# Performance work log

Hardware: AMD Instinct MI355X
Metric: run time of the kernel (lower is better)

The kernel has to match this reference:

```python
import jax, jax.numpy as jnp
import numpy as np


def setup_inputs() -> dict:
    key = jax.random.key(0)
    k1, k2 = jax.random.split(key)
    B, C, H, W = 4, 64, 256, 256
    x = jax.random.normal(k1, (B, C, H, W), dtype=jnp.float32)
    perspective = jax.random.uniform(k2, (B, 1, H, W), dtype=jnp.float32)
    alpha = jnp.ones((1,), dtype=jnp.float32) * 3.0   # sigma scale
    beta = jnp.ones((1,), dtype=jnp.float32)          # sigmoid slope
    gamma = jnp.zeros((1,), dtype=jnp.float32)        # sigmoid shift
    return {"x": x, "perspective": perspective, "alpha": alpha,
            "beta": beta, "gamma": gamma, "kernel_size": 7}


def reference(x, perspective, alpha, beta, gamma, kernel_size):
    K = int(kernel_size)
    pad = K // 2
    B, C, H, W = x.shape
    # AdaptiveSigmoid sigma map, clamped like the torch module
    sigma = jnp.maximum(alpha * jax.nn.sigmoid(beta * perspective + gamma), 1e-4)  # [B,1,H,W]
    inv2s2 = 1.0 / (2.0 * sigma * sigma)                                           # [B,1,H,W]
    # squared distance of each kernel tap from center (static)
    offs = np.arange(K) - pad
    d2 = (offs[:, None] ** 2 + offs[None, :] ** 2).reshape(-1).astype(np.float32)  # [K*K]
    # per-pixel, per-tap Gaussian weights, normalized over taps
    w = jnp.exp(-d2[:, None, None, None, None] * inv2s2[None])  # [K*K,B,1,H,W]
    w = w / jnp.sum(w, axis=0)
    xp = jnp.pad(x, ((0, 0), (0, 0), (pad, pad), (pad, pad)))
    out = jnp.zeros_like(x)
    k = 0
    for i in range(K):            # fixed small K*K loop (49 taps), jit-friendly
        for j in range(K):
            out = out + w[k] * xp[:, :, i:i + H, j:j + W]
            k += 1
    return out
```

## Files before the change

### kernel.cpp

```cpp
#include <hip/hip_runtime.h>

#define NB 4
#define NC 64
#define NH 256
#define NW 256
#define TH 32
#define SROWS (TH + 6)
#define LROW 256

__global__ __launch_bounds__(256)
void wprep(const float* __restrict__ persp,
           const float* __restrict__ alpha_p,
           const float* __restrict__ beta_p,
           const float* __restrict__ gamma_p,
           float* __restrict__ wg)
{
    const float alpha = alpha_p[0];
    const float beta  = beta_p[0];
    const float gamma = gamma_p[0];
    const int i = (blockIdx.x * 256 + threadIdx.x) * 4;
    const float4 p = *(const float4*)(persp + i);
    const float pa[4] = {p.x, p.y, p.z, p.w};
    float g[4];
    #pragma unroll
    for (int k = 0; k < 4; ++k) {
        const float z  = fmaf(beta, pa[k], gamma);
        const float sg = __builtin_amdgcn_rcpf(1.0f + __expf(-z));
        const float sigma = fmaxf(alpha * sg, 1e-4f);
        const float t  = 0.5f * __builtin_amdgcn_rcpf(sigma * sigma);
        g[k] = __expf(-t);
    }
    *(float4*)(wg + i) = make_float4(g[0], g[1], g[2], g[3]);
}

__device__ __forceinline__ float dpp_shr1(float v) {
    return __int_as_float(__builtin_amdgcn_update_dpp(
        0, __float_as_int(v), 0x138 , 0xf, 0xf, true));
}
__device__ __forceinline__ float dpp_shl1(float v) {
    return __int_as_float(__builtin_amdgcn_update_dpp(
        0, __float_as_int(v), 0x130 , 0xf, 0xf, true));
}

__global__ __launch_bounds__(256, 3)
void adaptive_gauss7(const float* __restrict__ x,
                     const float* __restrict__ wgp,
                     float* __restrict__ out)
{
    __shared__ float lds[SROWS * LROW];

    const int tid  = threadIdx.x;
    const int lane = tid & 63;
    const int wv   = tid >> 6;
    const int c    = blockIdx.x;
    const int h0   = blockIdx.y * TH;
    const int b    = blockIdx.z;
    const int colbase = lane * 4;
    const int rg      = h0 + wv * 8;

    const float* xc   = x   + (size_t)(b * NC + c) * NH * NW;
    float*       outp = out + (size_t)(b * NC + c) * NH * NW;
    const float* wrow = wgp + (size_t)b * NH * NW;

    float4 wsg[8];
    #pragma unroll
    for (int o = 0; o < 8; ++o)
        wsg[o] = *(const float4*)(wrow + (size_t)(rg + o) * NW + colbase);

    for (int r = wv; r < SROWS; r += 4) {
        const int gr = h0 - 3 + r;
        if ((unsigned)gr < NH) {
            __builtin_amdgcn_global_load_lds(
                (const __attribute__((address_space(1))) void*)(xc + (size_t)gr * NW + colbase),
                (__attribute__((address_space(3))) void*)&lds[r * LROW],
                16, 0, 0);
        } else {
            *(float4*)&lds[r * LROW + colbase] = make_float4(0.f, 0.f, 0.f, 0.f);
        }
    }
    __syncthreads();

    float win[7][4];
    #pragma unroll
    for (int r = 0; r < 7; ++r) {
        const float4 a = *(const float4*)&lds[(wv * 8 + r) * LROW + colbase];
        win[r][0] = a.x; win[r][1] = a.y; win[r][2] = a.z; win[r][3] = a.w;
    }

    #pragma unroll
    for (int o = 0; o < 8; ++o) {
        const float gk[4] = {wsg[o].x, wsg[o].y, wsg[o].z, wsg[o].w};
        float g[4], p4[4], p9[4], inv2[4];
        #pragma unroll
        for (int k = 0; k < 4; ++k) {
            g[k] = gk[k];
            const float g2 = g[k] * g[k];
            p4[k] = g2 * g2;
            p9[k] = p4[k] * p4[k] * g[k];
            const float S  = fmaf(2.0f, (g[k] + p4[k]) + p9[k], 1.0f);
            const float iv = __builtin_amdgcn_rcpf(S);
            inv2[k] = iv * iv;
        }

        float s0[4], s1[4], s2[4], s3[4];
        #pragma unroll
        for (int j = 0; j < 7; ++j) {
            const int s = (o + j) % 7;
            const float w[10] = {
                dpp_shr1(win[s][1]),
                dpp_shr1(win[s][2]),
                dpp_shr1(win[s][3]),
                win[s][0], win[s][1], win[s][2], win[s][3],
                dpp_shl1(win[s][0]),
                dpp_shl1(win[s][1]),
                dpp_shl1(win[s][2])
            };
            #pragma unroll
            for (int k = 0; k < 4; ++k) {
                const float rs = fmaf(p9[k], w[k]     + w[k + 6],
                                 fmaf(p4[k], w[k + 1] + w[k + 5],
                                 fmaf(g[k],  w[k + 2] + w[k + 4],
                                             w[k + 3])));
                if      (j == 0) s0[k] = rs;
                else if (j == 1) s1[k] = rs;
                else if (j == 2) s2[k] = rs;
                else if (j == 3) s3[k] = rs;
                else if (j == 4) s2[k] = s2[k] + rs;
                else if (j == 5) s1[k] = s1[k] + rs;
                else             s0[k] = s0[k] + rs;
            }
        }

        float res[4];
        #pragma unroll
        for (int k = 0; k < 4; ++k) {
            res[k] = fmaf(p9[k], s0[k],
                     fmaf(p4[k], s1[k],
                     fmaf(g[k],  s2[k], s3[k]))) * inv2[k];
        }
        *(float4*)(outp + (size_t)(rg + o) * NW + colbase) =
            make_float4(res[0], res[1], res[2], res[3]);

        if (o < 7) {
            const float4 a = *(const float4*)&lds[(wv * 8 + o + 7) * LROW + colbase];
            win[o % 7][0] = a.x; win[o % 7][1] = a.y;
            win[o % 7][2] = a.z; win[o % 7][3] = a.w;
        }
    }
}

extern "C" void kernel_launch(void* const* d_in, const int* in_sizes, int n_in,
                              void* d_out, int out_size, void* d_ws, size_t ws_size,
                              hipStream_t stream) {
    const float* x     = (const float*)d_in[0];
    const float* persp = (const float*)d_in[1];
    const float* alpha = (const float*)d_in[2];
    const float* beta  = (const float*)d_in[3];
    const float* gamma = (const float*)d_in[4];
    float* outp        = (float*)d_out;
    float* wg          = (float*)d_ws;

    wprep<<<dim3((NB * NH * NW) / 1024), dim3(256), 0, stream>>>(persp, alpha, beta, gamma, wg);
    adaptive_gauss7<<<dim3(NC, NH / TH, NB), dim3(256), 0, stream>>>(x, wg, outp);
}
```

Measured before the change: 136.1 us.

## Process several channels per block with double-buffered LDS staging

Each block now handles four channels instead of one. The next channel's tile is staged into a second LDS buffer with async global-to-LDS loads while the current channel is computed. The per-pixel Gaussian weights are loaded once and reused across those channels, which cuts redundant weight loads and per-block launch overhead. In exchange, LDS per block doubles, which limits blocks per CU, and the grid shrinks to a quarter as many blocks. The compiler may also insert conservative waits that serialize the prefetch.

```diff
diff --git a/kernel.cpp b/kernel.cpp
--- a/kernel.cpp
+++ b/kernel.cpp
@@ -4,6 +4,7 @@
 #define NC 64
 #define NH 256
 #define NW 256
+#define CPB 4
 #define TH 32
 #define SROWS (TH + 6)
 #define LROW 256
@@ -47,104 +48,118 @@
                      const float* __restrict__ wgp,
                      float* __restrict__ out)
 {
-    __shared__ float lds[SROWS * LROW];
+    __shared__ float lds[2][SROWS * LROW];
 
     const int tid  = threadIdx.x;
     const int lane = tid & 63;
     const int wv   = tid >> 6;
-    const int c    = blockIdx.x;
+    const int cg   = blockIdx.x;
     const int h0   = blockIdx.y * TH;
     const int b    = blockIdx.z;
     const int colbase = lane * 4;
     const int rg      = h0 + wv * 8;
+    const int c0      = cg * CPB;
 
-    const float* xc   = x   + (size_t)(b * NC + c) * NH * NW;
-    float*       outp = out + (size_t)(b * NC + c) * NH * NW;
+    const float* xb   = x   + (size_t)b * NC * NH * NW;
+    float*       outb = out + (size_t)b * NC * NH * NW;
     const float* wrow = wgp + (size_t)b * NH * NW;
+
+    auto stage = [&](int buf, int c) {
+        const float* xc = xb + (size_t)c * NH * NW;
+        for (int r = wv; r < SROWS; r += 4) {
+            const int gr = h0 - 3 + r;
+            if ((unsigned)gr < NH) {
+                __builtin_amdgcn_global_load_lds(
+                    (const __attribute__((address_space(1))) void*)(xc + (size_t)gr * NW + colbase),
+                    (__attribute__((address_space(3))) void*)&lds[buf][r * LROW],
+                    16, 0, 0);
+            } else {
+                *(float4*)&lds[buf][r * LROW + colbase] = make_float4(0.f, 0.f, 0.f, 0.f);
+            }
+        }
+    };
+
+    stage(0, c0);
 
     float4 wsg[8];
     #pragma unroll
     for (int o = 0; o < 8; ++o)
         wsg[o] = *(const float4*)(wrow + (size_t)(rg + o) * NW + colbase);
 
-    for (int r = wv; r < SROWS; r += 4) {
-        const int gr = h0 - 3 + r;
-        if ((unsigned)gr < NH) {
-            __builtin_amdgcn_global_load_lds(
-                (const __attribute__((address_space(1))) void*)(xc + (size_t)gr * NW + colbase),
-                (__attribute__((address_space(3))) void*)&lds[r * LROW],
-                16, 0, 0);
-        } else {
-            *(float4*)&lds[r * LROW + colbase] = make_float4(0.f, 0.f, 0.f, 0.f);
-        }
-    }
-    __syncthreads();
+    for (int ci = 0; ci < CPB; ++ci) {
+        __syncthreads();
+        if (ci + 1 < CPB)
+            stage((ci + 1) & 1, c0 + ci + 1);
 
-    float win[7][4];
-    #pragma unroll
-    for (int r = 0; r < 7; ++r) {
-        const float4 a = *(const float4*)&lds[(wv * 8 + r) * LROW + colbase];
-        win[r][0] = a.x; win[r][1] = a.y; win[r][2] = a.z; win[r][3] = a.w;
-    }
+        const float* ldsc = lds[ci & 1];
+        float*       outp = outb + (size_t)(c0 + ci) * NH * NW;
 
-    #pragma unroll
-    for (int o = 0; o < 8; ++o) {
-        const float gk[4] = {wsg[o].x, wsg[o].y, wsg[o].z, wsg[o].w};
-        float g[4], p4[4], p9[4], inv2[4];
+        float win[7][4];
         #pragma unroll
-        for (int k = 0; k < 4; ++k) {
-            g[k] = gk[k];
-            const float g2 = g[k] * g[k];
-            p4[k] = g2 * g2;
-            p9[k] = p4[k] * p4[k] * g[k];
-            const float S  = fmaf(2.0f, (g[k] + p4[k]) + p9[k], 1.0f);
-            const float iv = __builtin_amdgcn_rcpf(S);
-            inv2[k] = iv * iv;
+        for (int r = 0; r < 7; ++r) {
+            const float4 a = *(const float4*)&ldsc[(wv * 8 + r) * LROW + colbase];
+            win[r][0] = a.x; win[r][1] = a.y; win[r][2] = a.z; win[r][3] = a.w;
         }
 
-        float s0[4], s1[4], s2[4], s3[4];
         #pragma unroll
-        for (int j = 0; j < 7; ++j) {
-            const int s = (o + j) % 7;
-            const float w[10] = {
-                dpp_shr1(win[s][1]),
-                dpp_shr1(win[s][2]),
-                dpp_shr1(win[s][3]),
-                win[s][0], win[s][1], win[s][2], win[s][3],
-                dpp_shl1(win[s][0]),
-                dpp_shl1(win[s][1]),
-                dpp_shl1(win[s][2])
-            };
+        for (int o = 0; o < 8; ++o) {
+            const float gk[4] = {wsg[o].x, wsg[o].y, wsg[o].z, wsg[o].w};
+            float g[4], p4[4], p9[4], inv2[4];
             #pragma unroll
             for (int k = 0; k < 4; ++k) {
-                const float rs = fmaf(p9[k], w[k]     + w[k + 6],
-                                 fmaf(p4[k], w[k + 1] + w[k + 5],
-                                 fmaf(g[k],  w[k + 2] + w[k + 4],
-                                             w[k + 3])));
-                if      (j == 0) s0[k] = rs;
-                else if (j == 1) s1[k] = rs;
-                else if (j == 2) s2[k] = rs;
-                else if (j == 3) s3[k] = rs;
-                else if (j == 4) s2[k] = s2[k] + rs;
-                else if (j == 5) s1[k] = s1[k] + rs;
-                else             s0[k] = s0[k] + rs;
+                g[k] = gk[k];
+                const float g2 = g[k] * g[k];
+                p4[k] = g2 * g2;
+                p9[k] = p4[k] * p4[k] * g[k];
+                const float S  = fmaf(2.0f, (g[k] + p4[k]) + p9[k], 1.0f);
+                const float iv = __builtin_amdgcn_rcpf(S);
+                inv2[k] = iv * iv;
             }
-        }
 
-        float res[4];
-        #pragma unroll
-        for (int k = 0; k < 4; ++k) {
-            res[k] = fmaf(p9[k], s0[k],
-                     fmaf(p4[k], s1[k],
-                     fmaf(g[k],  s2[k], s3[k]))) * inv2[k];
-        }
-        *(float4*)(outp + (size_t)(rg + o) * NW + colbase) =
-            make_float4(res[0], res[1], res[2], res[3]);
+            float s0[4], s1[4], s2[4], s3[4];
+            #pragma unroll
+            for (int j = 0; j < 7; ++j) {
+                const int s = (o + j) % 7;
+                const float w[10] = {
+                    dpp_shr1(win[s][1]),
+                    dpp_shr1(win[s][2]),
+                    dpp_shr1(win[s][3]),
+                    win[s][0], win[s][1], win[s][2], win[s][3],
+                    dpp_shl1(win[s][0]),
+                    dpp_shl1(win[s][1]),
+                    dpp_shl1(win[s][2])
+                };
+                #pragma unroll
+                for (int k = 0; k < 4; ++k) {
+                    const float rs = fmaf(p9[k], w[k]     + w[k + 6],
+                                     fmaf(p4[k], w[k + 1] + w[k + 5],
+                                     fmaf(g[k],  w[k + 2] + w[k + 4],
+                                                 w[k + 3])));
+                    if      (j == 0) s0[k] = rs;
+                    else if (j == 1) s1[k] = rs;
+                    else if (j == 2) s2[k] = rs;
+                    else if (j == 3) s3[k] = rs;
+                    else if (j == 4) s2[k] = s2[k] + rs;
+                    else if (j == 5) s1[k] = s1[k] + rs;
+                    else             s0[k] = s0[k] + rs;
+                }
+            }
 
-        if (o < 7) {
-            const float4 a = *(const float4*)&lds[(wv * 8 + o + 7) * LROW + colbase];
-            win[o % 7][0] = a.x; win[o % 7][1] = a.y;
-            win[o % 7][2] = a.z; win[o % 7][3] = a.w;
+            float res[4];
+            #pragma unroll
+            for (int k = 0; k < 4; ++k) {
+                res[k] = fmaf(p9[k], s0[k],
+                         fmaf(p4[k], s1[k],
+                         fmaf(g[k],  s2[k], s3[k]))) * inv2[k];
+            }
+            *(float4*)(outp + (size_t)(rg + o) * NW + colbase) =
+                make_float4(res[0], res[1], res[2], res[3]);
+
+            if (o < 7) {
+                const float4 a = *(const float4*)&ldsc[(wv * 8 + o + 7) * LROW + colbase];
+                win[o % 7][0] = a.x; win[o % 7][1] = a.y;
+                win[o % 7][2] = a.z; win[o % 7][3] = a.w;
+            }
         }
     }
 }
@@ -161,5 +176,5 @@
     float* wg          = (float*)d_ws;
 
     wprep<<<dim3((NB * NH * NW) / 1024), dim3(256), 0, stream>>>(persp, alpha, beta, gamma, wg);
-    adaptive_gauss7<<<dim3(NC, NH / TH, NB), dim3(256), 0, stream>>>(x, wg, outp);
+    adaptive_gauss7<<<dim3(NC / CPB, NH / TH, NB), dim3(256), 0, stream>>>(x, wg, outp);
 }
```

Result: no change. 138.0 us (+1.4%).
